# Performance work log

Measured on AMD Instinct MI355X. Metric: run time of the kernel, lower is better.

## Reference

```python
import jax, jax.numpy as jnp
import numpy as np

NUM_HEADS = 12
MAX_REL = 64

def setup_inputs() -> dict:
    key = jax.random.key(0)
    k1, k2, k3, k4 = jax.random.split(key, 4)
    B, N, C = 4, 1024, 768
    x = jax.random.normal(k1, (B, N, C), dtype=jnp.float32)
    qkv_w = jax.random.normal(k2, (3 * C, C), dtype=jnp.float32) * 0.02
    proj_w = jax.random.normal(k3, (C, C), dtype=jnp.float32) * 0.02
    proj_b = jnp.zeros((C,), dtype=jnp.float32)
    rel_table = jax.random.normal(k4, (2 * MAX_REL + 1, NUM_HEADS), dtype=jnp.float32) * 0.02
    return {"x": x, "qkv_w": qkv_w, "proj_w": proj_w, "proj_b": proj_b, "rel_table": rel_table}

def reference(x, qkv_w, proj_w, proj_b, rel_table):
    B, N, C = x.shape
    H = NUM_HEADS
    D = C // H
    scale = D ** -0.5
    # qkv projection: (B,N,3C) -> (3,B,H,N,D)
    qkv = (x @ qkv_w.T).reshape(B, N, 3, H, D).transpose(2, 0, 3, 1, 4)
    q, k, v = qkv[0], qkv[1], qkv[2]
    attn = jnp.einsum('bhnd,bhmd->bhnm', q, k) * scale
    # relative position bias: clamp(j - i + MAX_REL, 0, 2*MAX_REL)
    idx = jnp.clip(jnp.arange(N)[None, :] - jnp.arange(N)[:, None] + MAX_REL, 0, 2 * MAX_REL)
    pos_bias = rel_table[idx]                      # (N,N,H)
    attn = attn + pos_bias.transpose(2, 0, 1)[None]  # (1,H,N,N)
    attn = jax.nn.softmax(attn, axis=-1)
    out = jnp.einsum('bhnm,bhmd->bnhd', attn, v).reshape(B, N, C)
    return out @ proj_w.T + proj_b
```

## Files before the change

kernel.cpp:

```cpp
#include <hip/hip_runtime.h>
#include <math.h>

#define HH 12
#define NN 1024

typedef unsigned int u32;
typedef unsigned short u16;
typedef __attribute__((ext_vector_type(8))) short bf16x8;
typedef __attribute__((ext_vector_type(4))) float f32x4;
typedef __attribute__((ext_vector_type(4))) unsigned short u16x4;

#define QSCALE 0.18033688f

__device__ __forceinline__ u16 bf16_rtn(float f) {
    u32 u = __builtin_bit_cast(u32, f);
    return (u16)((u + 0x7FFFu + ((u >> 16) & 1u)) >> 16);
}
__device__ __forceinline__ float bf16_up(u16 h) {
    u32 u = ((u32)h) << 16;
    return __builtin_bit_cast(float, u);
}
__device__ __forceinline__ void gld_lds16(const void* g, void* l) {
    __builtin_amdgcn_global_load_lds(
        (const __attribute__((address_space(1))) u32*)(unsigned long long)g,
        (__attribute__((address_space(3))) u32*)(u32)(unsigned long long)l,
        16, 0, 0);
}

__global__ __launch_bounds__(256) void presplit(const float* __restrict__ in,
                                                u16* __restrict__ hi, u16* __restrict__ lo,
                                                int n4) {
    int i = blockIdx.x * 256 + threadIdx.x;
    if (i >= n4) return;
    float4 v = ((const float4*)in)[i];
    float f[4] = {v.x, v.y, v.z, v.w};
    u16x4 h, l;
#pragma unroll
    for (int j = 0; j < 4; ++j) {
        u16 hh = bf16_rtn(f[j]);
        h[j] = hh;
        l[j] = bf16_rtn(f[j] - bf16_up(hh));
    }
    ((u16x4*)hi)[i] = h;
    ((u16x4*)lo)[i] = l;
}

__global__ __launch_bounds__(256) void gemm_qkv(const float* __restrict__ X,
                                                const u16* __restrict__ Wh,
                                                const u16* __restrict__ Wl,
                                                u16* __restrict__ qh, u16* __restrict__ ql,
                                                u16* __restrict__ kh, u16* __restrict__ kl,
                                                u16* __restrict__ vT) {
    __shared__ __align__(16) u16 sA[2][8][512];
    __shared__ __align__(16) u16 sB[2][8][512];

    const int tid = threadIdx.x, wave = tid >> 6, lane = tid & 63;
    const int g = lane >> 4, c = lane & 15;
    const int m0 = blockIdx.y * 128, c0 = blockIdx.x * 128;
    const int wm = wave >> 1, wn = wave & 1;

    f32x4 acc[4][4];
#pragma unroll
    for (int i = 0; i < 4; ++i)
#pragma unroll
        for (int j = 0; j < 4; ++j) acc[i][j] = (f32x4)(0.f);

    for (int k0 = 0; k0 < 768; k0 += 32) {
        __syncthreads();
#pragma unroll
        for (int qq = 0; qq < 4; ++qq) {
            const int idx = wave * 4 + qq;
            const int pl = idx >> 3, t = idx & 7;
            const u16* src = (pl ? Wl : Wh) + (size_t)(c0 + t * 16 + c) * 768 + k0 + g * 8;
            gld_lds16(src, &sB[pl][t][0]);
        }
#pragma unroll
        for (int tt = 0; tt < 2; ++tt) {
            const int t = wave * 2 + tt;
            const float* p = X + (size_t)(m0 + t * 16 + c) * 768 + k0 + g * 8;
            const float4 v0 = *(const float4*)p;
            const float4 v1 = *(const float4*)(p + 4);
            const float f[8] = {v0.x, v0.y, v0.z, v0.w, v1.x, v1.y, v1.z, v1.w};
            bf16x8 vh, vl;
#pragma unroll
            for (int e = 0; e < 8; ++e) {
                const u32 u = __builtin_bit_cast(u32, f[e]);
                const u16 hh = (u16)(u >> 16);
                const float r = f[e] - bf16_up(hh);
                vh[e] = (short)hh;
                vl[e] = (short)(__builtin_bit_cast(u32, r) >> 16);
            }
            *(bf16x8*)&sA[0][t][lane * 8] = vh;
            *(bf16x8*)&sA[1][t][lane * 8] = vl;
        }
        __syncthreads();

        bf16x8 Ah[4], Al[4], Bh[4], Bl[4];
#pragma unroll
        for (int i = 0; i < 4; ++i) {
            Ah[i] = *(const bf16x8*)&sA[0][wm * 4 + i][lane * 8];
            Al[i] = *(const bf16x8*)&sA[1][wm * 4 + i][lane * 8];
            Bh[i] = *(const bf16x8*)&sB[0][wn * 4 + i][lane * 8];
            Bl[i] = *(const bf16x8*)&sB[1][wn * 4 + i][lane * 8];
        }
#pragma unroll
        for (int i = 0; i < 4; ++i)
#pragma unroll
            for (int j = 0; j < 4; ++j) {
                acc[i][j] = __builtin_amdgcn_mfma_f32_16x16x32_bf16(Ah[i], Bh[j], acc[i][j], 0, 0, 0);
                acc[i][j] = __builtin_amdgcn_mfma_f32_16x16x32_bf16(Ah[i], Bl[j], acc[i][j], 0, 0, 0);
                acc[i][j] = __builtin_amdgcn_mfma_f32_16x16x32_bf16(Al[i], Bh[j], acc[i][j], 0, 0, 0);
            }
    }

    const int b = m0 >> 10;
#pragma unroll
    for (int j = 0; j < 4; ++j) {
        const int cg = c0 + wn * 64 + j * 16;
        const int s = cg / 768;
        const int h = (cg % 768) / 64;
        const int d = (cg % 64) + c;
#pragma unroll
        for (int i = 0; i < 4; ++i) {
            const int nbase = (m0 & 1023) + wm * 64 + i * 16 + g * 4;
            if (s == 2) {
                u16x4 pk;
#pragma unroll
                for (int r = 0; r < 4; ++r) pk[r] = bf16_rtn(acc[i][j][r]);
                *(u16x4*)(vT + ((size_t)(b * HH + h) << 16) + (size_t)d * 1024 + nbase) = pk;
            } else {
                u16* dh = s ? kh : qh;
                u16* dl = s ? kl : ql;
                const float sc = s ? 1.0f : QSCALE;
#pragma unroll
                for (int r = 0; r < 4; ++r) {
                    const float vv = acc[i][j][r] * sc;
                    const u16 hh = bf16_rtn(vv);
                    const size_t a = ((size_t)(b * HH + h) * NN + nbase + r) * 64 + d;
                    dh[a] = hh;
                    dl[a] = bf16_rtn(vv - bf16_up(hh));
                }
            }
        }
    }
}

__global__ __launch_bounds__(256) void attn_mfma(const u16* __restrict__ qh_,
                                                 const u16* __restrict__ ql_,
                                                 const u16* __restrict__ kh_,
                                                 const u16* __restrict__ kl_,
                                                 const u16* __restrict__ vT,
                                                 const float* __restrict__ rel_table,
                                                 u16* __restrict__ attout) {
    __shared__ __align__(16) u16 sK[2][4][2][512];
    __shared__ __align__(16) u16 sV[4][2][512];
    __shared__ __align__(16) u16 sP[4][32][72];
    __shared__ float tbl[132];

    const int tid = threadIdx.x, wave = tid >> 6, lane = tid & 63;
    const int g = lane >> 4, c = lane & 15;
    const int bh = blockIdx.x % 48;
    const int q0 = (blockIdx.x / 48) * 128;
    const int b = bh / HH, h = bh % HH;

    if (tid < 129) tbl[tid] = rel_table[tid * HH + h] * 1.44269504f;

    bf16x8 Qh[2][2], Ql[2][2];
#pragma unroll
    for (int rt = 0; rt < 2; ++rt)
#pragma unroll
        for (int ks = 0; ks < 2; ++ks) {
            const size_t a = ((size_t)bh * NN + q0 + wave * 32 + rt * 16 + c) * 64 + ks * 32 + g * 8;
            Qh[rt][ks] = *(const bf16x8*)(qh_ + a);
            Ql[rt][ks] = *(const bf16x8*)(ql_ + a);
        }

    f32x4 O[2][4];
    float mrun[2][4], lrun[2][4];
#pragma unroll
    for (int rt = 0; rt < 2; ++rt)
#pragma unroll
        for (int r = 0; r < 4; ++r) {
            mrun[rt][r] = -INFINITY;
            lrun[rt][r] = 0.f;
        }
#pragma unroll
    for (int rt = 0; rt < 2; ++rt)
#pragma unroll
        for (int dj = 0; dj < 4; ++dj) O[rt][dj] = (f32x4)(0.f);

    __syncthreads();

    for (int t = 0; t < 16; ++t) {
        const int kv0 = t * 64;
        __syncthreads();
#pragma unroll
        for (int qq = 0; qq < 6; ++qq) {
            const int idx = wave * 6 + qq;
            if (idx < 16) {
                const int pl = idx >> 3, rem = idx & 7, jn = rem >> 1, ks = rem & 1;
                const u16* src = (pl ? kl_ : kh_) + ((size_t)bh * NN + kv0 + jn * 16 + c) * 64 + ks * 32 + g * 8;
                gld_lds16(src, &sK[pl][jn][ks][0]);
            } else {
                const int rem = idx - 16, dj = rem >> 1, ks = rem & 1;
                const u16* src = vT + ((size_t)bh << 16) + (size_t)(dj * 16 + c) * 1024 + kv0 + ks * 32 + g * 8;
                gld_lds16(src, &sV[dj][ks][0]);
            }
        }
        __syncthreads();

        f32x4 S[2][4];
#pragma unroll
        for (int rt = 0; rt < 2; ++rt)
#pragma unroll
            for (int jn = 0; jn < 4; ++jn) S[rt][jn] = (f32x4)(0.f);
#pragma unroll
        for (int jn = 0; jn < 4; ++jn)
#pragma unroll
            for (int ks = 0; ks < 2; ++ks) {
                const bf16x8 Kh_ = *(const bf16x8*)&sK[0][jn][ks][lane * 8];
                const bf16x8 Kl_ = *(const bf16x8*)&sK[1][jn][ks][lane * 8];
#pragma unroll
                for (int rt = 0; rt < 2; ++rt) {
                    S[rt][jn] = __builtin_amdgcn_mfma_f32_16x16x32_bf16(Qh[rt][ks], Kh_, S[rt][jn], 0, 0, 0);
                    S[rt][jn] = __builtin_amdgcn_mfma_f32_16x16x32_bf16(Qh[rt][ks], Kl_, S[rt][jn], 0, 0, 0);
                    S[rt][jn] = __builtin_amdgcn_mfma_f32_16x16x32_bf16(Ql[rt][ks], Kh_, S[rt][jn], 0, 0, 0);
                }
            }

#pragma unroll
        for (int rt = 0; rt < 2; ++rt) {
            const int R0 = q0 + wave * 32 + rt * 16;
#pragma unroll
            for (int jn = 0; jn < 4; ++jn) {
                const int dd = (kv0 + jn * 16) - R0;
                if (dd <= -79) {
                    const float bv = tbl[0];
#pragma unroll
                    for (int r = 0; r < 4; ++r) S[rt][jn][r] += bv;
                } else if (dd >= 79) {
                    const float bv = tbl[128];
#pragma unroll
                    for (int r = 0; r < 4; ++r) S[rt][jn][r] += bv;
                } else {
#pragma unroll
                    for (int r = 0; r < 4; ++r) {
                        int off = dd + c - g * 4 - r + 64;
                        off = off < 0 ? 0 : (off > 128 ? 128 : off);
                        S[rt][jn][r] += tbl[off];
                    }
                }
            }
        }

#pragma unroll
        for (int rt = 0; rt < 2; ++rt) {
#pragma unroll
            for (int r = 0; r < 4; ++r) {
                float mx = fmaxf(fmaxf(S[rt][0][r], S[rt][1][r]), fmaxf(S[rt][2][r], S[rt][3][r]));
                mx = fmaxf(mx, __shfl_xor(mx, 1));
                mx = fmaxf(mx, __shfl_xor(mx, 2));
                mx = fmaxf(mx, __shfl_xor(mx, 4));
                mx = fmaxf(mx, __shfl_xor(mx, 8));
                const float mnew = fmaxf(mrun[rt][r], mx);
                const float alpha = exp2f(mrun[rt][r] - mnew);
                mrun[rt][r] = mnew;
                float rs = 0.f;
#pragma unroll
                for (int jn = 0; jn < 4; ++jn) {
                    const float p = exp2f(S[rt][jn][r] - mnew);
                    S[rt][jn][r] = p;
                    rs += p;
                }
                rs += __shfl_xor(rs, 1);
                rs += __shfl_xor(rs, 2);
                rs += __shfl_xor(rs, 4);
                rs += __shfl_xor(rs, 8);
                lrun[rt][r] = lrun[rt][r] * alpha + rs;
#pragma unroll
                for (int dj = 0; dj < 4; ++dj) O[rt][dj][r] *= alpha;
            }
        }

#pragma unroll
        for (int rt = 0; rt < 2; ++rt)
#pragma unroll
            for (int jn = 0; jn < 4; ++jn)
#pragma unroll
                for (int r = 0; r < 4; ++r)
                    sP[wave][rt * 16 + g * 4 + r][jn * 16 + c] = bf16_rtn(S[rt][jn][r]);

#pragma unroll
        for (int ks = 0; ks < 2; ++ks) {
            const bf16x8 Pa0 = *(const bf16x8*)&sP[wave][c][ks * 32 + g * 8];
            const bf16x8 Pa1 = *(const bf16x8*)&sP[wave][16 + c][ks * 32 + g * 8];
#pragma unroll
            for (int dj = 0; dj < 4; ++dj) {
                const bf16x8 Vf = *(const bf16x8*)&sV[dj][ks][lane * 8];
                O[0][dj] = __builtin_amdgcn_mfma_f32_16x16x32_bf16(Pa0, Vf, O[0][dj], 0, 0, 0);
                O[1][dj] = __builtin_amdgcn_mfma_f32_16x16x32_bf16(Pa1, Vf, O[1][dj], 0, 0, 0);
            }
        }
    }

#pragma unroll
    for (int rt = 0; rt < 2; ++rt)
#pragma unroll
        for (int r = 0; r < 4; ++r) {
            const float inv = 1.0f / lrun[rt][r];
            const int n = q0 + wave * 32 + rt * 16 + g * 4 + r;
            u16* dst = attout + (size_t)(b * NN + n) * 768 + h * 64;
#pragma unroll
            for (int dj = 0; dj < 4; ++dj)
                dst[dj * 16 + c] = bf16_rtn(O[rt][dj][r] * inv);
        }
}

__global__ __launch_bounds__(256) void gemm_proj(const u16* __restrict__ A,
                                                 const u16* __restrict__ Wh,
                                                 const u16* __restrict__ Wl,
                                                 const float* __restrict__ bias,
                                                 float* __restrict__ out) {
    __shared__ __align__(16) u16 sA[8][512];
    __shared__ __align__(16) u16 sB[2][8][512];

    const int tid = threadIdx.x, wave = tid >> 6, lane = tid & 63;
    const int g = lane >> 4, c = lane & 15;
    const int m0 = blockIdx.y * 128, c0 = blockIdx.x * 128;
    const int wm = wave >> 1, wn = wave & 1;

    f32x4 acc[4][4];
#pragma unroll
    for (int i = 0; i < 4; ++i)
#pragma unroll
        for (int j = 0; j < 4; ++j) acc[i][j] = (f32x4)(0.f);

    for (int k0 = 0; k0 < 768; k0 += 32) {
        __syncthreads();
#pragma unroll
        for (int qq = 0; qq < 6; ++qq) {
            const int idx = wave * 6 + qq;
            if (idx < 8) {
                const u16* src = A + (size_t)(m0 + idx * 16 + c) * 768 + k0 + g * 8;
                gld_lds16(src, &sA[idx][0]);
            } else {
                const int rem = idx - 8, pl = rem >> 3, tt = rem & 7;
                const u16* src = (pl ? Wl : Wh) + (size_t)(c0 + tt * 16 + c) * 768 + k0 + g * 8;
                gld_lds16(src, &sB[pl][tt][0]);
            }
        }
        __syncthreads();

        bf16x8 Aa[4], Bh[4], Bl[4];
#pragma unroll
        for (int i = 0; i < 4; ++i) {
            Aa[i] = *(const bf16x8*)&sA[wm * 4 + i][lane * 8];
            Bh[i] = *(const bf16x8*)&sB[0][wn * 4 + i][lane * 8];
            Bl[i] = *(const bf16x8*)&sB[1][wn * 4 + i][lane * 8];
        }
#pragma unroll
        for (int i = 0; i < 4; ++i)
#pragma unroll
            for (int j = 0; j < 4; ++j) {
                acc[i][j] = __builtin_amdgcn_mfma_f32_16x16x32_bf16(Aa[i], Bh[j], acc[i][j], 0, 0, 0);
                acc[i][j] = __builtin_amdgcn_mfma_f32_16x16x32_bf16(Aa[i], Bl[j], acc[i][j], 0, 0, 0);
            }
    }

#pragma unroll
    for (int j = 0; j < 4; ++j) {
        const int cg = c0 + wn * 64 + j * 16 + c;
        const float bv = bias[cg];
#pragma unroll
        for (int i = 0; i < 4; ++i)
#pragma unroll
            for (int r = 0; r < 4; ++r) {
                const int m = m0 + wm * 64 + i * 16 + g * 4 + r;
                out[(size_t)m * 768 + cg] = acc[i][j][r] + bv;
            }
    }
}

extern "C" void kernel_launch(void* const* d_in, const int* in_sizes, int n_in,
                              void* d_out, int out_size, void* d_ws, size_t ws_size,
                              hipStream_t stream) {
    const float* x = (const float*)d_in[0];
    const float* qkv_w = (const float*)d_in[1];
    const float* proj_w = (const float*)d_in[2];
    const float* proj_b = (const float*)d_in[3];
    const float* rel_table = (const float*)d_in[4];

    char* ws = (char*)d_ws;
    u16* qkvwh = (u16*)(ws);
    u16* qkvwl = (u16*)(ws + 3538944);
    u16* qh = (u16*)(ws + 7077888);
    u16* ql = (u16*)(ws + 13369344);
    u16* kh = (u16*)(ws + 19660800);
    u16* kl = (u16*)(ws + 25952256);
    u16* vT = (u16*)(ws + 32243712);
    u16* ao = (u16*)(ws + 38535168);
    u16* pwh = (u16*)(ws + 44826624);
    u16* pwl = (u16*)(ws + 46006272);

    presplit<<<dim3(1728), 256, 0, stream>>>(qkv_w, qkvwh, qkvwl, 442368);
    presplit<<<dim3(576), 256, 0, stream>>>(proj_w, pwh, pwl, 147456);

    gemm_qkv<<<dim3(18, 32), 256, 0, stream>>>(x, qkvwh, qkvwl, qh, ql, kh, kl, vT);

    attn_mfma<<<dim3(384), 256, 0, stream>>>(qh, ql, kh, kl, vT, rel_table, ao);

    gemm_proj<<<dim3(6, 32), 256, 0, stream>>>(ao, pwh, pwl, proj_b, (float*)d_out);
}
```

Measured before the change: 293.5 us.

## Presplit x, double-buffer GEMM LDS, swizzle tiles, shrink proj tiles, set MFMA priority

x is now split into bf16 hi/lo in a separate presplit kernel, so the QKV GEMM can load both operands with async global-to-LDS copies. Both GEMMs now use double-buffered LDS with one barrier per k-step, and blocks are remapped in a grouped order to improve L2 locality. The projection GEMM moves to 64x64 tiles to launch more blocks, and the attention kernel raises wave priority around its MFMA sections. This adds an extra kernel launch and traffic for the split x, reuses workspace regions, and changes the x high-part rounding from truncation to round-to-nearest.

```diff
diff --git a/kernel.cpp b/kernel.cpp
--- a/kernel.cpp
+++ b/kernel.cpp
@@ -45,18 +45,21 @@
     ((u16x4*)lo)[i] = l;
 }
 
-__global__ __launch_bounds__(256) void gemm_qkv(const float* __restrict__ X,
+__global__ __launch_bounds__(256) void gemm_qkv(const u16* __restrict__ Xh,
+                                                const u16* __restrict__ Xl,
                                                 const u16* __restrict__ Wh,
                                                 const u16* __restrict__ Wl,
                                                 u16* __restrict__ qh, u16* __restrict__ ql,
                                                 u16* __restrict__ kh, u16* __restrict__ kl,
                                                 u16* __restrict__ vT) {
-    __shared__ __align__(16) u16 sA[2][8][512];
-    __shared__ __align__(16) u16 sB[2][8][512];
+    __shared__ __align__(16) u16 sA[2][2][8][512];
+    __shared__ __align__(16) u16 sB[2][2][8][512];
 
     const int tid = threadIdx.x, wave = tid >> 6, lane = tid & 63;
     const int g = lane >> 4, c = lane & 15;
-    const int m0 = blockIdx.y * 128, c0 = blockIdx.x * 128;
+    const int bid = blockIdx.x;
+    const int T = (bid & 7) * 72 + (bid >> 3);
+    const int m0 = (T / 18) * 128, c0 = (T % 18) * 128;
     const int wm = wave >> 1, wn = wave & 1;
 
     f32x4 acc[4][4];
@@ -65,43 +68,35 @@
 #pragma unroll
         for (int j = 0; j < 4; ++j) acc[i][j] = (f32x4)(0.f);
 
-    for (int k0 = 0; k0 < 768; k0 += 32) {
+    auto stage = [&](int kt, int b) {
+#pragma unroll
+        for (int qq = 0; qq < 8; ++qq) {
+            const int id2 = wave * 8 + qq;
+            const int pl = (id2 >> 3) & 1;
+            const int t = id2 & 7;
+            if (id2 < 16) {
+                const u16* src = (pl ? Xl : Xh) + (size_t)(m0 + t * 16 + c) * 768 + kt * 32 + g * 8;
+                gld_lds16(src, &sA[b][pl][t][0]);
+            } else {
+                const u16* src = (pl ? Wl : Wh) + (size_t)(c0 + t * 16 + c) * 768 + kt * 32 + g * 8;
+                gld_lds16(src, &sB[b][pl][t][0]);
+            }
+        }
+    };
+
+    stage(0, 0);
+    for (int kt = 0; kt < 24; ++kt) {
+        const int b = kt & 1;
         __syncthreads();
-#pragma unroll
-        for (int qq = 0; qq < 4; ++qq) {
-            const int idx = wave * 4 + qq;
-            const int pl = idx >> 3, t = idx & 7;
-            const u16* src = (pl ? Wl : Wh) + (size_t)(c0 + t * 16 + c) * 768 + k0 + g * 8;
-            gld_lds16(src, &sB[pl][t][0]);
-        }
-#pragma unroll
-        for (int tt = 0; tt < 2; ++tt) {
-            const int t = wave * 2 + tt;
-            const float* p = X + (size_t)(m0 + t * 16 + c) * 768 + k0 + g * 8;
-            const float4 v0 = *(const float4*)p;
-            const float4 v1 = *(const float4*)(p + 4);
-            const float f[8] = {v0.x, v0.y, v0.z, v0.w, v1.x, v1.y, v1.z, v1.w};
-            bf16x8 vh, vl;
-#pragma unroll
-            for (int e = 0; e < 8; ++e) {
-                const u32 u = __builtin_bit_cast(u32, f[e]);
-                const u16 hh = (u16)(u >> 16);
-                const float r = f[e] - bf16_up(hh);
-                vh[e] = (short)hh;
-                vl[e] = (short)(__builtin_bit_cast(u32, r) >> 16);
-            }
-            *(bf16x8*)&sA[0][t][lane * 8] = vh;
-            *(bf16x8*)&sA[1][t][lane * 8] = vl;
-        }
-        __syncthreads();
+        if (kt < 23) stage(kt + 1, b ^ 1);
 
         bf16x8 Ah[4], Al[4], Bh[4], Bl[4];
 #pragma unroll
         for (int i = 0; i < 4; ++i) {
-            Ah[i] = *(const bf16x8*)&sA[0][wm * 4 + i][lane * 8];
-            Al[i] = *(const bf16x8*)&sA[1][wm * 4 + i][lane * 8];
-            Bh[i] = *(const bf16x8*)&sB[0][wn * 4 + i][lane * 8];
-            Bl[i] = *(const bf16x8*)&sB[1][wn * 4 + i][lane * 8];
+            Ah[i] = *(const bf16x8*)&sA[b][0][wm * 4 + i][lane * 8];
+            Al[i] = *(const bf16x8*)&sA[b][1][wm * 4 + i][lane * 8];
+            Bh[i] = *(const bf16x8*)&sB[b][0][wn * 4 + i][lane * 8];
+            Bl[i] = *(const bf16x8*)&sB[b][1][wn * 4 + i][lane * 8];
         }
 #pragma unroll
         for (int i = 0; i < 4; ++i)
@@ -214,6 +209,7 @@
         for (int rt = 0; rt < 2; ++rt)
 #pragma unroll
             for (int jn = 0; jn < 4; ++jn) S[rt][jn] = (f32x4)(0.f);
+        __builtin_amdgcn_s_setprio(1);
 #pragma unroll
         for (int jn = 0; jn < 4; ++jn)
 #pragma unroll
@@ -227,6 +223,7 @@
                     S[rt][jn] = __builtin_amdgcn_mfma_f32_16x16x32_bf16(Ql[rt][ks], Kh_, S[rt][jn], 0, 0, 0);
                 }
             }
+        __builtin_amdgcn_s_setprio(0);
 
 #pragma unroll
         for (int rt = 0; rt < 2; ++rt) {
@@ -290,6 +287,7 @@
                 for (int r = 0; r < 4; ++r)
                     sP[wave][rt * 16 + g * 4 + r][jn * 16 + c] = bf16_rtn(S[rt][jn][r]);
 
+        __builtin_amdgcn_s_setprio(1);
 #pragma unroll
         for (int ks = 0; ks < 2; ++ks) {
             const bf16x8 Pa0 = *(const bf16x8*)&sP[wave][c][ks * 32 + g * 8];
@@ -301,6 +299,7 @@
                 O[1][dj] = __builtin_amdgcn_mfma_f32_16x16x32_bf16(Pa1, Vf, O[1][dj], 0, 0, 0);
             }
         }
+        __builtin_amdgcn_s_setprio(0);
     }
 
 #pragma unroll
@@ -321,61 +320,68 @@
                                                  const u16* __restrict__ Wl,
                                                  const float* __restrict__ bias,
                                                  float* __restrict__ out) {
-    __shared__ __align__(16) u16 sA[8][512];
-    __shared__ __align__(16) u16 sB[2][8][512];
+    __shared__ __align__(16) u16 sA[2][4][512];
+    __shared__ __align__(16) u16 sB[2][2][4][512];
 
     const int tid = threadIdx.x, wave = tid >> 6, lane = tid & 63;
     const int g = lane >> 4, c = lane & 15;
-    const int m0 = blockIdx.y * 128, c0 = blockIdx.x * 128;
+    const int bid = blockIdx.x;
+    const int T = (bid & 7) * 96 + (bid >> 3);
+    const int m0 = (T / 12) * 64, c0 = (T % 12) * 64;
     const int wm = wave >> 1, wn = wave & 1;
 
-    f32x4 acc[4][4];
-#pragma unroll
-    for (int i = 0; i < 4; ++i)
-#pragma unroll
-        for (int j = 0; j < 4; ++j) acc[i][j] = (f32x4)(0.f);
-
-    for (int k0 = 0; k0 < 768; k0 += 32) {
+    f32x4 acc[2][2];
+#pragma unroll
+    for (int i = 0; i < 2; ++i)
+#pragma unroll
+        for (int j = 0; j < 2; ++j) acc[i][j] = (f32x4)(0.f);
+
+    auto stage = [&](int kt, int bb) {
+#pragma unroll
+        for (int qq = 0; qq < 3; ++qq) {
+            const int id2 = wave * 3 + qq;
+            if (id2 < 4) {
+                const u16* src = A + (size_t)(m0 + id2 * 16 + c) * 768 + kt * 32 + g * 8;
+                gld_lds16(src, &sA[bb][id2][0]);
+            } else {
+                const int rem = id2 - 4, pl = rem >> 2, t = rem & 3;
+                const u16* src = (pl ? Wl : Wh) + (size_t)(c0 + t * 16 + c) * 768 + kt * 32 + g * 8;
+                gld_lds16(src, &sB[bb][pl][t][0]);
+            }
+        }
+    };
+
+    stage(0, 0);
+    for (int kt = 0; kt < 24; ++kt) {
+        const int bb = kt & 1;
         __syncthreads();
-#pragma unroll
-        for (int qq = 0; qq < 6; ++qq) {
-            const int idx = wave * 6 + qq;
-            if (idx < 8) {
-                const u16* src = A + (size_t)(m0 + idx * 16 + c) * 768 + k0 + g * 8;
-                gld_lds16(src, &sA[idx][0]);
-            } else {
-                const int rem = idx - 8, pl = rem >> 3, tt = rem & 7;
-                const u16* src = (pl ? Wl : Wh) + (size_t)(c0 + tt * 16 + c) * 768 + k0 + g * 8;
-                gld_lds16(src, &sB[pl][tt][0]);
-            }
-        }
-        __syncthreads();
-
-        bf16x8 Aa[4], Bh[4], Bl[4];
-#pragma unroll
-        for (int i = 0; i < 4; ++i) {
-            Aa[i] = *(const bf16x8*)&sA[wm * 4 + i][lane * 8];
-            Bh[i] = *(const bf16x8*)&sB[0][wn * 4 + i][lane * 8];
-            Bl[i] = *(const bf16x8*)&sB[1][wn * 4 + i][lane * 8];
-        }
-#pragma unroll
-        for (int i = 0; i < 4; ++i)
-#pragma unroll
-            for (int j = 0; j < 4; ++j) {
+        if (kt < 23) stage(kt + 1, bb ^ 1);
+
+        bf16x8 Aa[2], Bh[2], Bl[2];
+#pragma unroll
+        for (int i = 0; i < 2; ++i) {
+            Aa[i] = *(const bf16x8*)&sA[bb][wm * 2 + i][lane * 8];
+            Bh[i] = *(const bf16x8*)&sB[bb][0][wn * 2 + i][lane * 8];
+            Bl[i] = *(const bf16x8*)&sB[bb][1][wn * 2 + i][lane * 8];
+        }
+#pragma unroll
+        for (int i = 0; i < 2; ++i)
+#pragma unroll
+            for (int j = 0; j < 2; ++j) {
                 acc[i][j] = __builtin_amdgcn_mfma_f32_16x16x32_bf16(Aa[i], Bh[j], acc[i][j], 0, 0, 0);
                 acc[i][j] = __builtin_amdgcn_mfma_f32_16x16x32_bf16(Aa[i], Bl[j], acc[i][j], 0, 0, 0);
             }
     }
 
 #pragma unroll
-    for (int j = 0; j < 4; ++j) {
-        const int cg = c0 + wn * 64 + j * 16 + c;
+    for (int j = 0; j < 2; ++j) {
+        const int cg = c0 + wn * 32 + j * 16 + c;
         const float bv = bias[cg];
 #pragma unroll
-        for (int i = 0; i < 4; ++i)
+        for (int i = 0; i < 2; ++i)
 #pragma unroll
             for (int r = 0; r < 4; ++r) {
-                const int m = m0 + wm * 64 + i * 16 + g * 4 + r;
+                const int m = m0 + wm * 32 + i * 16 + g * 4 + r;
                 out[(size_t)m * 768 + cg] = acc[i][j][r] + bv;
             }
     }
@@ -393,21 +399,25 @@
     char* ws = (char*)d_ws;
     u16* qkvwh = (u16*)(ws);
     u16* qkvwl = (u16*)(ws + 3538944);
-    u16* qh = (u16*)(ws + 7077888);
-    u16* ql = (u16*)(ws + 13369344);
-    u16* kh = (u16*)(ws + 19660800);
-    u16* kl = (u16*)(ws + 25952256);
-    u16* vT = (u16*)(ws + 32243712);
-    u16* ao = (u16*)(ws + 38535168);
-    u16* pwh = (u16*)(ws + 44826624);
-    u16* pwl = (u16*)(ws + 46006272);
-
+    u16* xh    = (u16*)(ws + 7077888);
+    u16* xl    = (u16*)(ws + 13369344);
+    u16* qh    = (u16*)(ws + 19660800);
+    u16* ql    = (u16*)(ws + 25952256);
+    u16* kh    = (u16*)(ws + 32243712);
+    u16* kl    = (u16*)(ws + 38535168);
+    u16* vT    = (u16*)(ws + 44826624);
+    u16* ao    = (u16*)(ws + 7077888);
+    u16* pwh   = (u16*)(ws + 13369344);
+    u16* pwl   = (u16*)(ws + 14548992);
+
+    presplit<<<dim3(3072), 256, 0, stream>>>(x, xh, xl, 786432);
     presplit<<<dim3(1728), 256, 0, stream>>>(qkv_w, qkvwh, qkvwl, 442368);
+
+    gemm_qkv<<<dim3(576), 256, 0, stream>>>(xh, xl, qkvwh, qkvwl, qh, ql, kh, kl, vT);
+
     presplit<<<dim3(576), 256, 0, stream>>>(proj_w, pwh, pwl, 147456);
 
-    gemm_qkv<<<dim3(18, 32), 256, 0, stream>>>(x, qkvwh, qkvwl, qh, ql, kh, kl, vT);
-
     attn_mfma<<<dim3(384), 256, 0, stream>>>(qh, ql, kh, kl, vT, rel_table, ao);
 
-    gemm_proj<<<dim3(6, 32), 256, 0, stream>>>(ao, pwh, pwl, proj_b, (float*)d_out);
-}
+    gemm_proj<<<dim3(768), 256, 0, stream>>>(ao, pwh, pwl, proj_b, (float*)d_out);
+}
```

After: 385.4 us. 31.3% more time.
